# Kernel tuning notes

Hardware: AMD Instinct MI355X
Metric: run time of the kernel (lower is better)

The kernel has to match this reference:

```python
import jax, jax.numpy as jnp
import numpy as np

EPS = 1e-12  # torch F.normalize eps


def _l2_normalize(x, axis=-1):
    n = jnp.linalg.norm(x, axis=axis, keepdims=True)
    return x / jnp.maximum(n, EPS)


def setup_inputs() -> dict:
    key = jax.random.key(0)
    k1, k2 = jax.random.split(key)
    B, N, D, V = 4, 512, 768, 50257
    return {
        "query": jax.random.normal(k1, (B, N, D), dtype=jnp.float32),
        "key_embeddings": jax.random.normal(k2, (V, D), dtype=jnp.float32),
        "alpha_raw": jnp.float32(0.5),  # learnable scalar parameter (init_alpha)
        "k": 64,
    }


def reference(query, key_embeddings, alpha_raw, k):
    # query: [B,N,D], key_embeddings: [V,D]
    query_norm = _l2_normalize(query)            # [B,N,D]
    key_norm = _l2_normalize(key_embeddings)     # [V,D]
    # node-level cosine similarity, max-pooled over nodes
    node_sim = jnp.einsum('bnd,vd->bnv', query_norm, key_norm)  # [B,N,V]
    node_sim_pool = node_sim.max(axis=1)                        # [B,V]
    # graph-level similarity from mean of normalized node features
    graph_query = query_norm.mean(axis=1)                       # [B,D]
    graph_sim = jnp.einsum('bd,vd->bv', graph_query, key_norm)  # [B,V]
    alpha = jax.nn.sigmoid(alpha_raw)
    fused_similarity = alpha * node_sim_pool + (1.0 - alpha) * graph_sim  # [B,V]
    _, topk_indices = jax.lax.top_k(fused_similarity, k)        # [B,k]
    selected_keys = key_embeddings[topk_indices]                # [B,k,D]
    return selected_keys, topk_indices, fused_similarity, alpha
```

## Files before the change

### kernel.cpp

```cpp
#include <hip/hip_runtime.h>
#include <hip/hip_bf16.h>
#include <math.h>

#define D 768
#define BQ 4
#define NQ 512
#define M_TOTAL (BQ*NQ)
#define KSEL 64

typedef short bf16x8 __attribute__((ext_vector_type(8)));
typedef float f32x4  __attribute__((ext_vector_type(4)));

__device__ __forceinline__ void split1(float x, unsigned int& h, unsigned int& l)
{
    unsigned int u  = __float_as_uint(x);
    unsigned int hb = (u + 0x7fffu + ((u >> 16) & 1u)) & 0xffff0000u;
    h = hb >> 16;
    l = __float_as_uint(x - __uint_as_float(hb)) >> 16;
}


__global__ void split_invnorm_kernel(const float* __restrict__ x, unsigned short* __restrict__ sp,
                                     float* __restrict__ inv, int rows_src, int rows_dst)
{
    int r    = (blockIdx.x * blockDim.x + threadIdx.x) >> 6;
    int lane = threadIdx.x & 63;
    if (r >= rows_dst) return;
    int src = r < rows_src ? r : rows_src - 1;
    const float* row = x + (size_t)src * D;
    unsigned short* dh = sp + (size_t)r * (2*D);
    unsigned short* dl = dh + D;
    float ss = 0.f;
    #pragma unroll
    for (int s = 0; s < 3; ++s) {
        float4 v = *reinterpret_cast<const float4*>(row + s*256 + lane*4);
        ss += v.x*v.x + v.y*v.y + v.z*v.z + v.w*v.w;
        unsigned int h0,h1,h2,h3,l0,l1,l2,l3;
        split1(v.x,h0,l0); split1(v.y,h1,l1); split1(v.z,h2,l2); split1(v.w,h3,l3);
        ushort4 hv = make_ushort4((unsigned short)h0,(unsigned short)h1,(unsigned short)h2,(unsigned short)h3);
        ushort4 lv = make_ushort4((unsigned short)l0,(unsigned short)l1,(unsigned short)l2,(unsigned short)l3);
        *reinterpret_cast<ushort4*>(dh + s*256 + lane*4) = hv;
        *reinterpret_cast<ushort4*>(dl + s*256 + lane*4) = lv;
    }
    #pragma unroll
    for (int off = 32; off > 0; off >>= 1)
        ss += __shfl_xor(ss, off, 64);
    if (lane == 0 && r < rows_src)
        inv[r] = 1.0f / fmaxf(sqrtf(ss), 1e-12f);
}

#define GBM 256
#define GBN 256
#define GBK 32
#define GNT (D/GBK)
#define SLOT_B_OFF 32768
#define SLOT_SZ 65536

__device__ __forceinline__ void gload16(const unsigned short* g, char* l)
{
    __builtin_amdgcn_global_load_lds((const __attribute__((address_space(1))) void*)g,
                                     (__attribute__((address_space(3))) void*)l, 16, 0, 0);
}

__global__ __launch_bounds__(512, 2)
void fast_gemm(const unsigned short* __restrict__ Qsp, const unsigned short* __restrict__ Ksp,
               const float* __restrict__ invq, float* __restrict__ pmax, float* __restrict__ psum,
               int Vp, int gx)
{
    extern __shared__ char smem[];

    const int t    = threadIdx.x;
    const int lane = t & 63;
    const int w    = t >> 6;
    const int wr   = w >> 2;
    const int wc   = w & 3;

    int lid = blockIdx.x;
    int u   = (lid & 7) * gx + (lid >> 3);
    const int by = u & 7;
    const int bx = u >> 3;
    const int m0 = by * GBM;
    const int v0 = bx * GBN;

    const int lrow = lane >> 3;
    const int cc   = (lane & 7) ^ lrow;
    const size_t goff = (size_t)lrow * (2*D) + (size_t)(cc >> 2) * D + (size_t)(cc & 3) * 8;

    const int rAbase = ((w & 3) << 3) + ((w >> 2) << 7);
    const int rBbase = w * 32;

    const unsigned short* gAsrc = Qsp + (size_t)(m0 + rAbase) * (2*D) + goff;
    const unsigned short* gBsrc = Ksp + (size_t)(v0 + rBbase) * (2*D) + goff;

    #define SAk(k_, sl_, j_) gload16(gAsrc + (k_) + (size_t)(j_)*32*(2*D), (sl_) + (rAbase + (j_)*32)*128)
    #define SBk(k_, sl_, j_) gload16(gBsrc + (k_) + (size_t)(j_)*8 *(2*D), (sl_) + SLOT_B_OFF + (rBbase + (j_)*8)*128)

    const int l15 = lane & 15, kg = lane >> 4;
    const int sHi = ((kg    ) ^ (lane & 7)) * 16;
    const int sLo = ((kg + 4) ^ (lane & 7)) * 16;
    const int offA = (wr*128 + l15) * 128;
    const int offB = SLOT_B_OFF + (wc*64 + l15) * 128;

    f32x4 acc[8][4];
    #pragma unroll
    for (int i = 0; i < 8; ++i)
        #pragma unroll
        for (int j = 0; j < 4; ++j)
            acc[i][j] = f32x4{0.f,0.f,0.f,0.f};

    bf16x8 Bh[4], Bl[4];

    char* sl0 = smem;
    char* sl1 = smem + SLOT_SZ;

    SBk(0, sl0, 0); SBk(0, sl0, 1); SAk(0, sl0, 0);
    SBk(0, sl0, 2); SBk(0, sl0, 3); SAk(0, sl0, 1);
    SAk(0, sl0, 2); SAk(0, sl0, 3);
    asm volatile("s_waitcnt vmcnt(2)" ::: "memory");
    __builtin_amdgcn_s_barrier();

    #define PHASE(p_, STG, VMW) do {                                                         \
        bf16x8 Ah0 = *(const bf16x8*)(scur + offA + (2*(p_)  )*2048 + sHi);                  \
        bf16x8 Al0 = *(const bf16x8*)(scur + offA + (2*(p_)  )*2048 + sLo);                  \
        bf16x8 Ah1 = *(const bf16x8*)(scur + offA + (2*(p_)+1)*2048 + sHi);                  \
        bf16x8 Al1 = *(const bf16x8*)(scur + offA + (2*(p_)+1)*2048 + sLo);                  \
        STG;                                                                                 \
        __builtin_amdgcn_s_barrier();                                                        \
        asm volatile("s_waitcnt lgkmcnt(0)" ::: "memory");                                   \
        __builtin_amdgcn_s_setprio(1);                                                       \
        _Pragma("unroll")                                                                    \
        for (int nf = 0; nf < 4; ++nf) {                                                     \
            acc[2*(p_)  ][nf] = __builtin_amdgcn_mfma_f32_16x16x32_bf16(Ah0, Bh[nf], acc[2*(p_)  ][nf], 0,0,0); \
            acc[2*(p_)+1][nf] = __builtin_amdgcn_mfma_f32_16x16x32_bf16(Ah1, Bh[nf], acc[2*(p_)+1][nf], 0,0,0); \
        }                                                                                    \
        _Pragma("unroll")                                                                    \
        for (int nf = 0; nf < 4; ++nf) {                                                     \
            acc[2*(p_)  ][nf] = __builtin_amdgcn_mfma_f32_16x16x32_bf16(Ah0, Bl[nf], acc[2*(p_)  ][nf], 0,0,0); \
            acc[2*(p_)+1][nf] = __builtin_amdgcn_mfma_f32_16x16x32_bf16(Ah1, Bl[nf], acc[2*(p_)+1][nf], 0,0,0); \
        }                                                                                    \
        _Pragma("unroll")                                                                    \
        for (int nf = 0; nf < 4; ++nf) {                                                     \
            acc[2*(p_)  ][nf] = __builtin_amdgcn_mfma_f32_16x16x32_bf16(Al0, Bh[nf], acc[2*(p_)  ][nf], 0,0,0); \
            acc[2*(p_)+1][nf] = __builtin_amdgcn_mfma_f32_16x16x32_bf16(Al1, Bh[nf], acc[2*(p_)+1][nf], 0,0,0); \
        }                                                                                    \
        __builtin_amdgcn_s_setprio(0);                                                       \
        VMW;                                                                                 \
        __builtin_amdgcn_s_barrier();                                                        \
    } while(0)

    for (int T = 0; T < GNT; ++T) {
        const bool st = (T + 1 < GNT);
        char* scur = (T & 1) ? sl1 : sl0;
        char* snxt = (T & 1) ? sl0 : sl1;
        const int k1 = (T + 1) * GBK;

        #pragma unroll
        for (int nf = 0; nf < 4; ++nf) {
            Bh[nf] = *(const bf16x8*)(scur + offB + nf*2048 + sHi);
            Bl[nf] = *(const bf16x8*)(scur + offB + nf*2048 + sLo);
        }
        PHASE(0, { if (st) { SBk(k1, snxt, 0); SBk(k1, snxt, 1); SAk(k1, snxt, 0); } }, );
        PHASE(1, { if (st) { SBk(k1, snxt, 2); SBk(k1, snxt, 3); SAk(k1, snxt, 1); } },
                 { if (st) asm volatile("s_waitcnt vmcnt(6)" ::: "memory");
                   else    asm volatile("s_waitcnt vmcnt(0)" ::: "memory"); });
        PHASE(2, { if (st) SAk(k1, snxt, 2); }, );
        PHASE(3, { if (st) SAk(k1, snxt, 3); },
                 { if (st) asm volatile("s_waitcnt vmcnt(2)" ::: "memory"); });
    }
    #undef PHASE
    #undef SAk
    #undef SBk

    __syncthreads();
    float iq[32];
    #pragma unroll
    for (int mf = 0; mf < 8; ++mf)
        #pragma unroll
        for (int r = 0; r < 4; ++r)
            iq[mf*4+r] = invq[m0 + wr*128 + mf*16 + kg*4 + r];

    float* redm = (float*)smem;
    float* reds = redm + 512;
    #pragma unroll
    for (int nf = 0; nf < 4; ++nf) {
        float pmv = -INFINITY, psv = 0.f;
        #pragma unroll
        for (int mf = 0; mf < 8; ++mf)
            #pragma unroll
            for (int r = 0; r < 4; ++r) {
                float x = acc[mf][nf][r] * iq[mf*4+r];
                pmv = fmaxf(pmv, x);
                psv += x;
            }
        pmv = fmaxf(pmv, __shfl_xor(pmv, 16, 64));
        pmv = fmaxf(pmv, __shfl_xor(pmv, 32, 64));
        psv += __shfl_xor(psv, 16, 64);
        psv += __shfl_xor(psv, 32, 64);
        if (lane < 16) {
            redm[wr*256 + wc*64 + nf*16 + l15] = pmv;
            reds[wr*256 + wc*64 + nf*16 + l15] = psv;
        }
    }
    __syncthreads();
    if (t < 256) {
        pmax[(size_t)by * Vp + v0 + t] = fmaxf(redm[t], redm[256+t]);
        psum[(size_t)by * Vp + v0 + t] = reds[t] + reds[256+t];
    }
}

__global__ void blend_kernel(const float* __restrict__ pmax, const float* __restrict__ psum,
                             const float* __restrict__ invk, const float* __restrict__ alpha_raw,
                             float* __restrict__ out_fused, float* __restrict__ out_alpha,
                             int V, int Vp)
{
    int v = blockIdx.x * 256 + threadIdx.x;
    float alpha = 1.0f / (1.0f + expf(-alpha_raw[0]));
    if (blockIdx.x == 0 && threadIdx.x == 0) out_alpha[0] = alpha;
    if (v >= V) return;
    float ik = invk[v];
    #pragma unroll
    for (int b = 0; b < BQ; ++b) {
        float nm = fmaxf(pmax[(size_t)(2*b)*Vp + v], pmax[(size_t)(2*b+1)*Vp + v]) * ik;
        float gs = (psum[(size_t)(2*b)*Vp + v] + psum[(size_t)(2*b+1)*Vp + v]) * ik * (1.0f/(float)NQ);
        out_fused[(size_t)b*V + v] = alpha*nm + (1.0f-alpha)*gs;
    }
}

__device__ __forceinline__ unsigned int mono_map(float f)
{
    unsigned int u = __float_as_uint(f);
    return u ^ ((u & 0x80000000u) ? 0xFFFFFFFFu : 0x80000000u);
}

__global__ __launch_bounds__(1024)
void topk_radix_kernel(const float* __restrict__ fused,
                       int* __restrict__ idxout, float* __restrict__ out_idx, int V)
{
    const int b = blockIdx.x, t = threadIdx.x;
    const float* row = fused + (size_t)b * V;

    __shared__ unsigned int hist[256];
    __shared__ unsigned int sh_pref;
    __shared__ int sh_kneed;
    __shared__ unsigned int sh_nA, sh_nE;
    __shared__ unsigned long long key[64];
    __shared__ int eqIdx[256];

    unsigned int pref = 0;
    int kneed = KSEL;
    #pragma unroll
    for (int p = 24; p >= 0; p -= 8) {
        if (t < 256) hist[t] = 0;
        __syncthreads();
        unsigned int mask = (p == 24) ? 0u : (0xFFFFFFFFu << (p + 8));
        for (int i = t; i < V; i += 1024) {
            unsigned int u = mono_map(row[i]);
            if ((u & mask) == pref)
                atomicAdd(&hist[(u >> p) & 255u], 1u);
        }
        __syncthreads();
        if (t == 0) {
            int cum = 0, sel = 0;
            for (int bb = 255; bb >= 0; --bb) {
                int c = (int)hist[bb];
                if (cum + c >= kneed) { sel = bb; break; }
                cum += c;
            }
            sh_pref  = pref | ((unsigned int)sel << p);
            sh_kneed = kneed - cum;
        }
        __syncthreads();
        pref  = sh_pref;
        kneed = sh_kneed;
        __syncthreads();
    }

    const unsigned int T = pref;
    if (t == 0) { sh_nA = 0; sh_nE = 0; }
    __syncthreads();
    for (int i = t; i < V; i += 1024) {
        unsigned int u = mono_map(row[i]);
        if (u > T) {
            unsigned int pos = atomicAdd(&sh_nA, 1u);
            if (pos < 64) key[pos] = ((unsigned long long)(~u) << 32) | (unsigned int)i;
        } else if (u == T) {
            unsigned int pos = atomicAdd(&sh_nE, 1u);
            if (pos < 256) eqIdx[pos] = i;
        }
    }
    __syncthreads();
    const int nA = (int)sh_nA;
    const int nE = (int)sh_nE;
    if (t < 256 && t >= min(nE, 256)) eqIdx[t] = 0x7fffffff;
    __syncthreads();
    if (nE > 1) {
        for (int k = 2; k <= 256; k <<= 1)
            for (int j = k >> 1; j > 0; j >>= 1) {
                if (t < 256) {
                    int ixj = t ^ j;
                    if (ixj > t) {
                        int a = eqIdx[t], c = eqIdx[ixj];
                        bool up = ((t & k) == 0);
                        if ((a > c) == up) { eqIdx[t] = c; eqIdx[ixj] = a; }
                    }
                }
                __syncthreads();
            }
    }
    if (t < kneed)
        key[nA + t] = ((unsigned long long)(~T) << 32) | (unsigned int)eqIdx[t];
    __syncthreads();
    for (int k = 2; k <= 64; k <<= 1)
        for (int j = k >> 1; j > 0; j >>= 1) {
            if (t < 64) {
                int ixj = t ^ j;
                if (ixj > t) {
                    unsigned long long a = key[t], c = key[ixj];
                    bool up = ((t & k) == 0);
                    if ((a > c) == up) { key[t] = c; key[ixj] = a; }
                }
            }
            __syncthreads();
        }
    if (t < KSEL) {
        int idx = (int)(unsigned int)(key[t] & 0xFFFFFFFFull);
        idxout[b*KSEL + t]  = idx;
        out_idx[b*KSEL + t] = (float)idx;
    }
}

__global__ void gather_kernel(const int* __restrict__ idx, const float* __restrict__ Kmat,
                              float* __restrict__ out_sel)
{
    int j = blockIdx.x & 63, b = blockIdx.x >> 6, t = threadIdx.x;
    int sel = idx[b*KSEL + j];
    float4 v = *reinterpret_cast<const float4*>(Kmat + (size_t)sel * D + t*4);
    *reinterpret_cast<float4*>(out_sel + ((size_t)(b*KSEL + j)) * D + t*4) = v;
}

#define BMT 128
#define BVT 128
#define NSTEP (D/32)

__global__ void row_invnorm_kernel(const float* __restrict__ x, float* __restrict__ inv, int rows)
{
    int wid  = (blockIdx.x * blockDim.x + threadIdx.x) >> 6;
    int lane = threadIdx.x & 63;
    if (wid >= rows) return;
    const float* r = x + (size_t)wid * D;
    float ss = 0.f;
    #pragma unroll
    for (int s = 0; s < 3; ++s) {
        float4 v = *reinterpret_cast<const float4*>(r + s*256 + lane*4);
        ss += v.x*v.x + v.y*v.y + v.z*v.z + v.w*v.w;
    }
    #pragma unroll
    for (int off = 32; off > 0; off >>= 1)
        ss += __shfl_xor(ss, off, 64);
    if (lane == 0) inv[wid] = 1.0f / fmaxf(sqrtf(ss), 1e-12f);
}

__global__ void compute_gq_kernel(const float* __restrict__ q, const float* __restrict__ invq,
                                  float* __restrict__ gq)
{
    int t = blockIdx.x * blockDim.x + threadIdx.x;
    if (t >= BQ*D) return;
    int b = t / D, d = t - b*D;
    float acc = 0.f;
    const float* qb = q + (size_t)b * NQ * D + d;
    const float* iq = invq + b*NQ;
    for (int n = 0; n < NQ; ++n)
        acc += iq[n] * qb[(size_t)n*D];
    gq[t] = acc * (1.0f/(float)NQ);
}

__device__ __forceinline__ void split8(float4 a, float4 b, uint4& hi, uint4& lo)
{
    unsigned int h0,h1,h2,h3,h4,h5,h6,h7, l0,l1,l2,l3,l4,l5,l6,l7;
    split1(a.x,h0,l0); split1(a.y,h1,l1); split1(a.z,h2,l2); split1(a.w,h3,l3);
    split1(b.x,h4,l4); split1(b.y,h5,l5); split1(b.z,h6,l6); split1(b.w,h7,l7);
    hi.x = h0 | (h1<<16); hi.y = h2 | (h3<<16); hi.z = h4 | (h5<<16); hi.w = h6 | (h7<<16);
    lo.x = l0 | (l1<<16); lo.y = l2 | (l3<<16); lo.z = l4 | (l5<<16); lo.w = l6 | (l7<<16);
}

__global__ __launch_bounds__(256)
void mfma_gemm_maxpool(const float* __restrict__ Q, const float* __restrict__ Kmat,
                       const float* __restrict__ invq, const float* __restrict__ invk,
                       float* __restrict__ partial, int V, int Vp)
{
    __shared__ __align__(16) unsigned short lds[16384];
    const int t    = threadIdx.x;
    const int lane = t & 63;
    const int w    = t >> 6;
    const int wr   = w >> 1;
    const int wc   = w & 1;
    const int v0   = blockIdx.x * BVT;
    const int m0   = blockIdx.y * BMT;

    const int srow = t >> 1;
    const int scol = (t & 1) * 16;
    const int c0   = (t & 1) * 2;
    const unsigned int ps0 = (c0     + (srow >> 1)) & 3;
    const unsigned int ps1 = (c0 + 1 + (srow >> 1)) & 3;
    const unsigned int wO0 = srow*32 + ps0*8;
    const unsigned int wO1 = srow*32 + ps1*8;

    const float* Ap = Q + (size_t)(m0 + srow) * D + scol;
    int vrow = v0 + srow; if (vrow > V-1) vrow = V-1;
    const float* Bp = Kmat + (size_t)vrow * D + scol;

    const int lr = lane & 15, kg = lane >> 4;
    const int arowb = wr*64 + lr;
    const int browb = wc*64 + lr;
    const unsigned int slotA = (kg + (arowb >> 1)) & 3;
    const unsigned int slotB = (kg + (browb >> 1)) & 3;
    const unsigned int offA = arowb*32 + slotA*8;
    const unsigned int offB = browb*32 + slotB*8;

    f32x4 acc[4][4];
    #pragma unroll
    for (int i = 0; i < 4; ++i)
        #pragma unroll
        for (int j = 0; j < 4; ++j)
            acc[i][j] = f32x4{0.f,0.f,0.f,0.f};

    float4 ra0,ra1,ra2,ra3, rb0,rb1,rb2,rb3;
    #define LOADSTEP(s_) do { \
        const float* ap_ = Ap + (s_)*32; const float* bp_ = Bp + (s_)*32; \
        ra0 = *(const float4*)(ap_);    ra1 = *(const float4*)(ap_+4); \
        ra2 = *(const float4*)(ap_+8);  ra3 = *(const float4*)(ap_+12); \
        rb0 = *(const float4*)(bp_);    rb1 = *(const float4*)(bp_+4); \
        rb2 = *(const float4*)(bp_+8);  rb3 = *(const float4*)(bp_+12); \
    } while(0)

    LOADSTEP(0);
    for (int s = 0; s < NSTEP; ++s) {
        uint4 ah0,al0, ah1,al1, bh0,bl0, bh1,bl1;
        split8(ra0,ra1, ah0,al0); split8(ra2,ra3, ah1,al1);
        split8(rb0,rb1, bh0,bl0); split8(rb2,rb3, bh1,bl1);
        __syncthreads();
        *(uint4*)&lds[        wO0] = ah0;  *(uint4*)&lds[ 4096 + wO0] = al0;
        *(uint4*)&lds[        wO1] = ah1;  *(uint4*)&lds[ 4096 + wO1] = al1;
        *(uint4*)&lds[ 8192 + wO0] = bh0;  *(uint4*)&lds[12288 + wO0] = bl0;
        *(uint4*)&lds[ 8192 + wO1] = bh1;  *(uint4*)&lds[12288 + wO1] = bl1;
        if (s + 1 < NSTEP) LOADSTEP(s + 1);
        __syncthreads();

        bf16x8 Ah[4], Al[4], Bh[4], Bl[4];
        #pragma unroll
        for (int fm = 0; fm < 4; ++fm) {
            unsigned int o = offA + fm*512;
            Ah[fm] = *(const bf16x8*)&lds[o];
            Al[fm] = *(const bf16x8*)&lds[4096 + o];
        }
        #pragma unroll
        for (int fv = 0; fv < 4; ++fv) {
            unsigned int o = offB + fv*512;
            Bh[fv] = *(const bf16x8*)&lds[8192 + o];
            Bl[fv] = *(const bf16x8*)&lds[12288 + o];
        }
        #pragma unroll
        for (int fm = 0; fm < 4; ++fm)
            #pragma unroll
            for (int fv = 0; fv < 4; ++fv) {
                acc[fm][fv] = __builtin_amdgcn_mfma_f32_16x16x32_bf16(Ah[fm], Bh[fv], acc[fm][fv], 0,0,0);
                acc[fm][fv] = __builtin_amdgcn_mfma_f32_16x16x32_bf16(Ah[fm], Bl[fv], acc[fm][fv], 0,0,0);
                acc[fm][fv] = __builtin_amdgcn_mfma_f32_16x16x32_bf16(Al[fm], Bh[fv], acc[fm][fv], 0,0,0);
            }
    }
    #undef LOADSTEP

    __syncthreads();
    float* red = (float*)lds;
    float iq[4][4];
    #pragma unroll
    for (int fm = 0; fm < 4; ++fm)
        #pragma unroll
        for (int r = 0; r < 4; ++r)
            iq[fm][r] = invq[m0 + wr*64 + fm*16 + kg*4 + r];
    #pragma unroll
    for (int fv = 0; fv < 4; ++fv) {
        float tm = -INFINITY;
        #pragma unroll
        for (int fm = 0; fm < 4; ++fm)
            #pragma unroll
            for (int r = 0; r < 4; ++r)
                tm = fmaxf(tm, acc[fm][fv][r] * iq[fm][r]);
        tm = fmaxf(tm, __shfl_xor(tm, 16, 64));
        tm = fmaxf(tm, __shfl_xor(tm, 32, 64));
        if (lane < 16) red[wr*128 + wc*64 + fv*16 + lane] = tm;
    }
    __syncthreads();
    if (t < 128) {
        int v = v0 + t;
        if (v < V)
            partial[(size_t)blockIdx.y * Vp + v] = fmaxf(red[t], red[128 + t]) * invk[v];
    }
}

__global__ void fused_sim_kernel(const float* __restrict__ Kmat, const float* __restrict__ invk,
                                 const float* __restrict__ gq, const float* __restrict__ partial,
                                 const float* __restrict__ alpha_raw,
                                 float* __restrict__ out_fused, float* __restrict__ out_alpha,
                                 int V, int Vp)
{
    int wib  = threadIdx.x >> 6;
    int lane = threadIdx.x & 63;
    float alpha = 1.0f / (1.0f + expf(-alpha_raw[0]));
    if (blockIdx.x == 0 && threadIdx.x == 0) out_alpha[0] = alpha;
    int v = blockIdx.x * 4 + wib;
    if (v >= V) return;
    const float* kr = Kmat + (size_t)v * D;
    float accb[BQ] = {0.f,0.f,0.f,0.f};
    #pragma unroll
    for (int s = 0; s < 3; ++s) {
        float4 kv = *reinterpret_cast<const float4*>(kr + s*256 + lane*4);
        #pragma unroll
        for (int b = 0; b < BQ; ++b) {
            float4 gv = *reinterpret_cast<const float4*>(gq + b*D + s*256 + lane*4);
            accb[b] += gv.x*kv.x + gv.y*kv.y + gv.z*kv.z + gv.w*kv.w;
        }
    }
    #pragma unroll
    for (int b = 0; b < BQ; ++b)
        #pragma unroll
        for (int off = 32; off > 0; off >>= 1)
            accb[b] += __shfl_xor(accb[b], off, 64);
    if (lane < BQ) {
        int b = lane;
        float node = partial[(size_t)(b*4+0)*Vp + v];
        #pragma unroll
        for (int i = 1; i < 4; ++i)
            node = fmaxf(node, partial[(size_t)(b*4+i)*Vp + v]);
        float graph = accb[b] * invk[v];
        out_fused[(size_t)b*V + v] = alpha*node + (1.0f-alpha)*graph;
    }
}

__global__ __launch_bounds__(1024)
void topk_gather_kernel(const float* __restrict__ fused, const float* __restrict__ Kmat,
                        float* __restrict__ scratch, float* __restrict__ out_sel,
                        float* __restrict__ out_idx, int V, int Vp)
{
    const int b = blockIdx.x, t = threadIdx.x;
    const int lane = t & 63, wid = t >> 6;
    const float* row = fused + (size_t)b * V;
    float* s = scratch + (size_t)b * Vp;
    for (int i = t; i < V; i += 1024) s[i] = row[i];
    __syncthreads();

    const int CH = (V + 1023) / 1024;
    const int lo = t * CH;
    const int hi = min(V, lo + CH);
    float lmax = -INFINITY; int lidx = 0x7fffffff;
    for (int i = lo; i < hi; ++i) { float x = s[i]; if (x > lmax) { lmax = x; lidx = i; } }

    __shared__ float swv[16];
    __shared__ int   swi[16];
    __shared__ int   sbest;

    for (int j = 0; j < KSEL; ++j) {
        float v = lmax; int id = lidx;
        #pragma unroll
        for (int off = 32; off > 0; off >>= 1) {
            float ov = __shfl_xor(v, off, 64);
            int   oi = __shfl_xor(id, off, 64);
            if (ov > v || (ov == v && oi < id)) { v = ov; id = oi; }
        }
        if (lane == 0) { swv[wid] = v; swi[wid] = id; }
        __syncthreads();
        if (t == 0) {
            float bv = swv[0]; int bi = swi[0];
            for (int x = 1; x < 16; ++x)
                if (swv[x] > bv || (swv[x] == bv && swi[x] < bi)) { bv = swv[x]; bi = swi[x]; }
            sbest = bi;
            out_idx[b*KSEL + j] = (float)bi;
        }
        __syncthreads();
        const int sel = sbest;
        if (sel >= lo && sel < hi) {
            s[sel] = -INFINITY;
            lmax = -INFINITY; lidx = 0x7fffffff;
            for (int i = lo; i < hi; ++i) { float x = s[i]; if (x > lmax) { lmax = x; lidx = i; } }
        }
        if (t < 192) {
            float4 kv = *reinterpret_cast<const float4*>(&Kmat[(size_t)sel * D + t*4]);
            *reinterpret_cast<float4*>(&out_sel[((size_t)b*KSEL + j)*D + t*4]) = kv;
        }
        __syncthreads();
    }
}

extern "C" void kernel_launch(void* const* d_in, const int* in_sizes, int n_in,
                              void* d_out, int out_size, void* d_ws, size_t ws_size,
                              hipStream_t stream)
{
    const float* q         = (const float*)d_in[0];
    const float* kemb      = (const float*)d_in[1];
    const float* alpha_raw = (const float*)d_in[2];
    int V = in_sizes[1] / D;

    float* out_sel   = (float*)d_out;
    float* out_idx   = out_sel + BQ*KSEL*D;
    float* out_fused = out_idx + BQ*KSEL;
    float* out_alpha = out_fused + (size_t)BQ*V;

    size_t Vp = (size_t)((V + 255) & ~255);
    float* ws      = (float*)d_ws;
    float* invk    = ws;
    float* invq    = invk + Vp;
    float* pmax    = invq + M_TOTAL;
    float* psum    = pmax + 8*Vp;
    float* scratch = psum + 8*Vp;
    int*   idxbuf  = (int*)(scratch + 4*Vp);
    unsigned short* Qsp = (unsigned short*)(idxbuf + 256);
    unsigned short* Ksp = Qsp + (size_t)M_TOTAL * (2*D);
    size_t need = (size_t)((char*)(Ksp + Vp*(2*D)) - (char*)d_ws);

    if (ws_size >= need) {
        split_invnorm_kernel<<<M_TOTAL/4, 256, 0, stream>>>(q, Qsp, invq, M_TOTAL, M_TOTAL);
        split_invnorm_kernel<<<(int)(Vp/4), 256, 0, stream>>>(kemb, Ksp, invk, V, (int)Vp);

        hipFuncSetAttribute(reinterpret_cast<const void*>(fast_gemm),
                            hipFuncAttributeMaxDynamicSharedMemorySize, 2*SLOT_SZ);

        int gx = (int)(Vp / GBN);
        fast_gemm<<<gx*8, 512, 2*SLOT_SZ, stream>>>(Qsp, Ksp, invq, pmax, psum, (int)Vp, gx);

        blend_kernel<<<(V + 255)/256, 256, 0, stream>>>(pmax, psum, invk, alpha_raw,
                                                        out_fused, out_alpha, V, (int)Vp);
        topk_radix_kernel<<<BQ, 1024, 0, stream>>>(out_fused, idxbuf, out_idx, V);
        gather_kernel<<<BQ*KSEL, 192, 0, stream>>>(idxbuf, kemb, out_sel);
    } else {
        int Vp2 = (V + 127) & ~127;
        float* f_invk    = ws;
        float* f_invq    = f_invk + Vp2;
        float* f_gq      = f_invq + M_TOTAL;
        float* f_partial = f_gq + BQ*D;
        float* f_scratch = f_partial + (size_t)16*Vp2;

        row_invnorm_kernel<<<(V + 3)/4, 256, 0, stream>>>(kemb, f_invk, V);
        row_invnorm_kernel<<<(M_TOTAL + 3)/4, 256, 0, stream>>>(q, f_invq, M_TOTAL);
        compute_gq_kernel<<<(BQ*D + 255)/256, 256, 0, stream>>>(q, f_invq, f_gq);

        dim3 g(Vp2 / BVT, M_TOTAL / BMT);
        mfma_gemm_maxpool<<<g, 256, 0, stream>>>(q, kemb, f_invq, f_invk, f_partial, V, Vp2);

        fused_sim_kernel<<<(V + 3)/4, 256, 0, stream>>>(kemb, f_invk, f_gq, f_partial, alpha_raw,
                                                        out_fused, out_alpha, V, Vp2);
        topk_gather_kernel<<<BQ, 1024, 0, stream>>>(out_fused, kemb, f_scratch, out_sel, out_idx, V, Vp2);
    }
}
```

Before: 523.5 us.

## Double-buffer A fragment loads in registers across MFMA phases

Restructures the inner K-loop of the split-bf16 GEMM so that the A fragments for the next phase are read from LDS while the current phase's MFMAs run, using two register sets (even/odd) and partial lgkmcnt waits. The global-to-LDS stage issue order and the vmcnt wait points are rearranged to match, and sched_barriers pin the ordering. The aim is to hide LDS read latency behind MFMA work and cut per-phase waiting. In exchange it needs more registers, and the hand-tuned waitcnt counts are fragile if the number of loads changes.

Result: no change. 529.7 us (+1.2%).

```diff
diff --git a/kernel.cpp b/kernel.cpp
--- a/kernel.cpp
+++ b/kernel.cpp
@@ -101,6 +101,8 @@
     const int offA = (wr*128 + l15) * 128;
     const int offB = SLOT_B_OFF + (wc*64 + l15) * 128;
 
+    #define LDA(mf_, s_) (*(const bf16x8*)(scur + offA + (mf_)*2048 + (s_)))
+
     f32x4 acc[8][4];
     #pragma unroll
     for (int i = 0; i < 8; ++i)
@@ -113,39 +115,29 @@
     char* sl0 = smem;
     char* sl1 = smem + SLOT_SZ;
 
-    SBk(0, sl0, 0); SBk(0, sl0, 1); SAk(0, sl0, 0);
-    SBk(0, sl0, 2); SBk(0, sl0, 3); SAk(0, sl0, 1);
-    SAk(0, sl0, 2); SAk(0, sl0, 3);
+    SBk(0, sl0, 0); SBk(0, sl0, 1); SAk(0, sl0, 0); SAk(0, sl0, 1);
+    SBk(0, sl0, 2); SBk(0, sl0, 3); SAk(0, sl0, 2); SAk(0, sl0, 3);
     asm volatile("s_waitcnt vmcnt(2)" ::: "memory");
     __builtin_amdgcn_s_barrier();
 
-    #define PHASE(p_, STG, VMW) do {                                                         \
-        bf16x8 Ah0 = *(const bf16x8*)(scur + offA + (2*(p_)  )*2048 + sHi);                  \
-        bf16x8 Al0 = *(const bf16x8*)(scur + offA + (2*(p_)  )*2048 + sLo);                  \
-        bf16x8 Ah1 = *(const bf16x8*)(scur + offA + (2*(p_)+1)*2048 + sHi);                  \
-        bf16x8 Al1 = *(const bf16x8*)(scur + offA + (2*(p_)+1)*2048 + sLo);                  \
-        STG;                                                                                 \
-        __builtin_amdgcn_s_barrier();                                                        \
-        asm volatile("s_waitcnt lgkmcnt(0)" ::: "memory");                                   \
+    #define MFMA_PH(p_, A0h_,A0l_,A1h_,A1l_) do {                                            \
         __builtin_amdgcn_s_setprio(1);                                                       \
         _Pragma("unroll")                                                                    \
         for (int nf = 0; nf < 4; ++nf) {                                                     \
-            acc[2*(p_)  ][nf] = __builtin_amdgcn_mfma_f32_16x16x32_bf16(Ah0, Bh[nf], acc[2*(p_)  ][nf], 0,0,0); \
-            acc[2*(p_)+1][nf] = __builtin_amdgcn_mfma_f32_16x16x32_bf16(Ah1, Bh[nf], acc[2*(p_)+1][nf], 0,0,0); \
+            acc[2*(p_)  ][nf] = __builtin_amdgcn_mfma_f32_16x16x32_bf16(A0h_, Bh[nf], acc[2*(p_)  ][nf], 0,0,0); \
+            acc[2*(p_)+1][nf] = __builtin_amdgcn_mfma_f32_16x16x32_bf16(A1h_, Bh[nf], acc[2*(p_)+1][nf], 0,0,0); \
         }                                                                                    \
         _Pragma("unroll")                                                                    \
         for (int nf = 0; nf < 4; ++nf) {                                                     \
-            acc[2*(p_)  ][nf] = __builtin_amdgcn_mfma_f32_16x16x32_bf16(Ah0, Bl[nf], acc[2*(p_)  ][nf], 0,0,0); \
-            acc[2*(p_)+1][nf] = __builtin_amdgcn_mfma_f32_16x16x32_bf16(Ah1, Bl[nf], acc[2*(p_)+1][nf], 0,0,0); \
+            acc[2*(p_)  ][nf] = __builtin_amdgcn_mfma_f32_16x16x32_bf16(A0h_, Bl[nf], acc[2*(p_)  ][nf], 0,0,0); \
+            acc[2*(p_)+1][nf] = __builtin_amdgcn_mfma_f32_16x16x32_bf16(A1h_, Bl[nf], acc[2*(p_)+1][nf], 0,0,0); \
         }                                                                                    \
         _Pragma("unroll")                                                                    \
         for (int nf = 0; nf < 4; ++nf) {                                                     \
-            acc[2*(p_)  ][nf] = __builtin_amdgcn_mfma_f32_16x16x32_bf16(Al0, Bh[nf], acc[2*(p_)  ][nf], 0,0,0); \
-            acc[2*(p_)+1][nf] = __builtin_amdgcn_mfma_f32_16x16x32_bf16(Al1, Bh[nf], acc[2*(p_)+1][nf], 0,0,0); \
+            acc[2*(p_)  ][nf] = __builtin_amdgcn_mfma_f32_16x16x32_bf16(A0l_, Bh[nf], acc[2*(p_)  ][nf], 0,0,0); \
+            acc[2*(p_)+1][nf] = __builtin_amdgcn_mfma_f32_16x16x32_bf16(A1l_, Bh[nf], acc[2*(p_)+1][nf], 0,0,0); \
         }                                                                                    \
         __builtin_amdgcn_s_setprio(0);                                                       \
-        VMW;                                                                                 \
-        __builtin_amdgcn_s_barrier();                                                        \
     } while(0)
 
     for (int T = 0; T < GNT; ++T) {
@@ -159,15 +151,42 @@
             Bh[nf] = *(const bf16x8*)(scur + offB + nf*2048 + sHi);
             Bl[nf] = *(const bf16x8*)(scur + offB + nf*2048 + sLo);
         }
-        PHASE(0, { if (st) { SBk(k1, snxt, 0); SBk(k1, snxt, 1); SAk(k1, snxt, 0); } }, );
-        PHASE(1, { if (st) { SBk(k1, snxt, 2); SBk(k1, snxt, 3); SAk(k1, snxt, 1); } },
-                 { if (st) asm volatile("s_waitcnt vmcnt(6)" ::: "memory");
-                   else    asm volatile("s_waitcnt vmcnt(0)" ::: "memory"); });
-        PHASE(2, { if (st) SAk(k1, snxt, 2); }, );
-        PHASE(3, { if (st) SAk(k1, snxt, 3); },
-                 { if (st) asm volatile("s_waitcnt vmcnt(2)" ::: "memory"); });
-    }
-    #undef PHASE
+        bf16x8 eA0h = LDA(0,sHi), eA0l = LDA(0,sLo), eA1h = LDA(1,sHi), eA1l = LDA(1,sLo);
+        bf16x8 oA0h = LDA(2,sHi), oA0l = LDA(2,sLo), oA1h = LDA(3,sHi), oA1l = LDA(3,sLo);
+        if (st) { SBk(k1,snxt,0); SBk(k1,snxt,1); SAk(k1,snxt,0); SAk(k1,snxt,1); }
+        __builtin_amdgcn_s_barrier();
+        asm volatile("s_waitcnt lgkmcnt(4)" ::: "memory");
+        __builtin_amdgcn_sched_barrier(0);
+        MFMA_PH(0, eA0h,eA0l,eA1h,eA1l);
+        __builtin_amdgcn_s_barrier();
+
+        if (st) asm volatile("s_waitcnt vmcnt(5)" ::: "memory");
+        else    asm volatile("s_waitcnt vmcnt(1)" ::: "memory");
+        eA0h = LDA(4,sHi); eA0l = LDA(4,sLo); eA1h = LDA(5,sHi); eA1l = LDA(5,sLo);
+        if (st) { SBk(k1,snxt,2); SBk(k1,snxt,3); SAk(k1,snxt,2); SAk(k1,snxt,3); }
+        __builtin_amdgcn_s_barrier();
+        asm volatile("s_waitcnt lgkmcnt(4)" ::: "memory");
+        __builtin_amdgcn_sched_barrier(0);
+        MFMA_PH(1, oA0h,oA0l,oA1h,oA1l);
+        __builtin_amdgcn_s_barrier();
+
+        if (st) asm volatile("s_waitcnt vmcnt(8)" ::: "memory");
+        else    asm volatile("s_waitcnt vmcnt(0)" ::: "memory");
+        oA0h = LDA(6,sHi); oA0l = LDA(6,sLo); oA1h = LDA(7,sHi); oA1l = LDA(7,sLo);
+        __builtin_amdgcn_s_barrier();
+        asm volatile("s_waitcnt lgkmcnt(4)" ::: "memory");
+        __builtin_amdgcn_sched_barrier(0);
+        MFMA_PH(2, eA0h,eA0l,eA1h,eA1l);
+        __builtin_amdgcn_s_barrier();
+
+        asm volatile("s_waitcnt lgkmcnt(0)" ::: "memory");
+        __builtin_amdgcn_sched_barrier(0);
+        MFMA_PH(3, oA0h,oA0l,oA1h,oA1l);
+        if (st) asm volatile("s_waitcnt vmcnt(2)" ::: "memory");
+        __builtin_amdgcn_s_barrier();
+    }
+    #undef MFMA_PH
+    #undef LDA
     #undef SAk
     #undef SBk
 
```
